# Kernel tuning notes

Measured on AMD Instinct MI355X. Metric: run time of the kernel, lower is better.

Reference implementation:

```python
import jax, jax.numpy as jnp
import numpy as np

N_EMBD = 1024
HEAD_SIZE = 64


def setup_inputs() -> dict:
    key = jax.random.key(0)
    ks = jax.random.split(key, 7)
    B, T, C, H = 4, 4096, N_EMBD, HEAD_SIZE
    s = 1.0 / np.sqrt(C)
    return {
        "x": jax.random.normal(ks[0], (B, T, C), dtype=jnp.float32),
        "Wk": jax.random.uniform(ks[1], (C, H), jnp.float32, -s, s),
        "bk": jax.random.uniform(ks[2], (H,), jnp.float32, -s, s),
        "Wq": jax.random.uniform(ks[3], (C, H), jnp.float32, -s, s),
        "bq": jax.random.uniform(ks[4], (H,), jnp.float32, -s, s),
        "Wv": jax.random.uniform(ks[5], (C, H), jnp.float32, -s, s),
        "bv": jax.random.uniform(ks[6], (H,), jnp.float32, -s, s),
    }


def reference(x, Wk, bk, Wq, bq, Wv, bv):
    B, T, C = x.shape
    k = x @ Wk + bk  # [B,T,H]
    q = x @ Wq + bq
    v = x @ Wv + bv
    scale = k.shape[-1] ** -0.5
    wei = jnp.einsum("bth,bsh->bts", q, k) * scale  # [B,T,T]
    causal = jnp.tril(jnp.ones((T, T), dtype=bool))
    wei = jnp.where(causal, wei, -jnp.inf)
    wei = jax.nn.softmax(wei, axis=-1)
    return jnp.einsum("bts,bsh->bth", wei, v)
```

## Files before the change

kernel.cpp:

```cpp
#include <hip/hip_runtime.h>
#include <hip/hip_bf16.h>


typedef _Float16 f16;
typedef f16 half4 __attribute__((ext_vector_type(4)));
typedef f16 half8 __attribute__((ext_vector_type(8)));
typedef float f32x4 __attribute__((ext_vector_type(4)));

#define T_SEQ 4096
#define QSCL 0.1803368801111204f

__device__ __forceinline__ f32x4 mfma16(half8 a, half8 b, f32x4 c) {
    return __builtin_amdgcn_mfma_f32_16x16x32_f16(a, b, c, 0, 0, 0);
}

__global__ __launch_bounds__(256) void prep_w(const float* __restrict__ Wq,
                                              const float* __restrict__ Wk,
                                              const float* __restrict__ Wv,
                                              f16* __restrict__ Wfrag) {
    int nt = blockIdx.x;
    int mat = nt >> 2;
    const float* W = (mat == 0) ? Wq : (mat == 1 ? Wk : Wv);
    float s = (mat == 0) ? QSCL : 1.0f;
    int tid = threadIdx.x;
    int lane = tid & 63, g = lane >> 4, c16 = lane & 15;
    int ksb = (tid >> 6) * 8;
    int h = ((nt & 3) << 4) + c16;
#pragma unroll
    for (int q = 0; q < 8; ++q) {
        int ks = ksb + q;
        half8 o;
#pragma unroll
        for (int j = 0; j < 8; ++j) {
            int k = ks * 32 + g * 8 + j;
            o[j] = (f16)(W[(size_t)k * 64 + h] * s);
        }
        *reinterpret_cast<half8*>(&Wfrag[((size_t)(nt * 32 + ks) * 64 + lane) * 8]) = o;
    }
}

__global__ __launch_bounds__(256, 4) void proj(const float* __restrict__ x,
                                               const f16* __restrict__ Wfrag,
                                               const float* __restrict__ bk,
                                               const float* __restrict__ bq,
                                               const float* __restrict__ bv,
                                               f16* __restrict__ Qb, f16* __restrict__ Kb,
                                               f16* __restrict__ Vbt) {
    __shared__ f16 xs[16][1032];
    int m0 = blockIdx.x << 4;
    int tid = threadIdx.x;
    int w = tid >> 6, lane = tid & 63, g = lane >> 4, c16 = lane & 15;
    {
        int row = tid >> 4;
        int c0 = (tid & 15) << 2;
        const float* xr = &x[(size_t)(m0 + row) * 1024 + c0];
#pragma unroll
        for (int chunk = 0; chunk < 8; ++chunk) {
            float4 A = *reinterpret_cast<const float4*>(xr + chunk * 128);
            float4 B = *reinterpret_cast<const float4*>(xr + chunk * 128 + 64);
            half4 ha, hb;
            ha[0] = (f16)A.x; ha[1] = (f16)A.y; ha[2] = (f16)A.z; ha[3] = (f16)A.w;
            hb[0] = (f16)B.x; hb[1] = (f16)B.y; hb[2] = (f16)B.z; hb[3] = (f16)B.w;
            *reinterpret_cast<half4*>(&xs[row][c0 + chunk * 128]) = ha;
            *reinterpret_cast<half4*>(&xs[row][c0 + chunk * 128 + 64]) = hb;
        }
    }
    __syncthreads();
    f32x4 zero = {0.f, 0.f, 0.f, 0.f};
    f32x4 acc[3];
#pragma unroll
    for (int i = 0; i < 3; ++i) acc[i] = zero;
    const f16* wbase = &Wfrag[(size_t)(w * 3) * 32 * 64 * 8 + (size_t)lane * 8];
#pragma unroll 8
    for (int ks = 0; ks < 32; ++ks) {
        half8 a = *reinterpret_cast<const half8*>(&xs[c16][ks * 32 + g * 8]);
#pragma unroll
        for (int i = 0; i < 3; ++i) {
            half8 bf = *reinterpret_cast<const half8*>(
                wbase + ((size_t)i * 32 + ks) * 64 * 8);
            acc[i] = mfma16(a, bf, acc[i]);
        }
    }
    int b = m0 >> 12;
#pragma unroll
    for (int i = 0; i < 3; ++i) {
        int nt = w * 3 + i;
        int mat = nt >> 2;
        int h = ((nt & 3) << 4) + c16;
        float bias = (mat == 0) ? bq[h] * QSCL : (mat == 1 ? bk[h] : bv[h]);
#pragma unroll
        for (int j = 0; j < 4; ++j) {
            int row = m0 + g * 4 + j;
            f16 val = (f16)(acc[i][j] + bias);
            if (mat == 0) Qb[(size_t)row * 64 + h] = val;
            else if (mat == 1) Kb[(size_t)row * 64 + h] = val;
            else Vbt[((size_t)(b * 64 + h)) * 4096 + (row & 4095)] = val;
        }
    }
}

__global__ __launch_bounds__(256) void attn(const f16* __restrict__ Qb,
                                            const f16* __restrict__ Kb,
                                            const f16* __restrict__ Vbt,
                                            f16* __restrict__ Opart,
                                            float* __restrict__ Ml) {
    int rem = 287 - (int)blockIdx.x;
    int qt = 0, ck = 0;
    for (int bd = 0; bd < 8; ++bd) {
        int cnt = 8 * (bd + 1);
        if (rem < cnt) { qt = bd * 8 + rem / (bd + 1); ck = rem % (bd + 1); break; }
        rem -= cnt;
    }
    int b = blockIdx.y;
    int t0 = ck << 3;
    int nIter = min(8, qt + 1 - t0);
    int q0 = qt << 6;
    const f16* Q = Qb + (size_t)b * T_SEQ * 64;
    const f16* K = Kb + (size_t)b * T_SEQ * 64;
    const f16* Vg = Vbt + (size_t)b * 64 * T_SEQ;
    int tid = threadIdx.x;
    int w = tid >> 6, lane = tid & 63, g = lane >> 4, c16 = lane & 15;
    __shared__ f16 Kt[2][64][72];
    __shared__ f16 Vt[2][64][72];
    __shared__ f16 Pl[4][16][72];

    int qr = q0 + 16 * w + c16;
    half8 qf0 = *reinterpret_cast<const half8*>(&Q[(size_t)qr * 64 + g * 8]);
    half8 qf1 = *reinterpret_cast<const half8*>(&Q[(size_t)qr * 64 + 32 + g * 8]);

    f32x4 zero = {0.f, 0.f, 0.f, 0.f};
    f32x4 oacc[4];
#pragma unroll
    for (int i = 0; i < 4; ++i) oacc[i] = zero;
    float m_run = -__builtin_inff(), l_run = 0.f;

    int sr = tid >> 2, sc = (tid & 3) << 4;
    int k0 = t0 << 6;
    half8 kr0 = *reinterpret_cast<const half8*>(&K[(size_t)(k0 + sr) * 64 + sc]);
    half8 kr1 = *reinterpret_cast<const half8*>(&K[(size_t)(k0 + sr) * 64 + sc + 8]);
    half8 vr0 = *reinterpret_cast<const half8*>(&Vg[(size_t)sr * T_SEQ + k0 + sc]);
    half8 vr1 = *reinterpret_cast<const half8*>(&Vg[(size_t)sr * T_SEQ + k0 + sc + 8]);
    *reinterpret_cast<half8*>(&Kt[0][sr][sc]) = kr0;
    *reinterpret_cast<half8*>(&Kt[0][sr][sc + 8]) = kr1;
    *reinterpret_cast<half8*>(&Vt[0][sr][sc]) = vr0;
    *reinterpret_cast<half8*>(&Vt[0][sr][sc + 8]) = vr1;
    __syncthreads();
    int cur = 0;

    for (int it = 0; it < nIter; ++it) {
        int gt = t0 + it;
        if (it + 1 < nIter) {
            int kn = (gt + 1) << 6;
            kr0 = *reinterpret_cast<const half8*>(&K[(size_t)(kn + sr) * 64 + sc]);
            kr1 = *reinterpret_cast<const half8*>(&K[(size_t)(kn + sr) * 64 + sc + 8]);
            vr0 = *reinterpret_cast<const half8*>(&Vg[(size_t)sr * T_SEQ + kn + sc]);
            vr1 = *reinterpret_cast<const half8*>(&Vg[(size_t)sr * T_SEQ + kn + sc + 8]);
        }
        f32x4 st[4];
#pragma unroll
        for (int nt = 0; nt < 4; ++nt) st[nt] = zero;
#pragma unroll
        for (int nt = 0; nt < 4; ++nt) {
            half8 kf0 = *reinterpret_cast<const half8*>(&Kt[cur][nt * 16 + c16][g * 8]);
            half8 kf1 = *reinterpret_cast<const half8*>(&Kt[cur][nt * 16 + c16][32 + g * 8]);
            st[nt] = mfma16(kf0, qf0, st[nt]);
            st[nt] = mfma16(kf1, qf1, st[nt]);
        }
        if (gt == qt) {
            int kb = gt << 6;
#pragma unroll
            for (int nt = 0; nt < 4; ++nt)
#pragma unroll
                for (int jj = 0; jj < 4; ++jj)
                    if (kb + nt * 16 + g * 4 + jj > qr) st[nt][jj] = -1e30f;
        }
        float mx;
        {
            f32x4 e01 = __builtin_elementwise_max(st[0], st[1]);
            f32x4 e23 = __builtin_elementwise_max(st[2], st[3]);
            f32x4 e = __builtin_elementwise_max(e01, e23);
            mx = fmaxf(fmaxf(e[0], e[1]), fmaxf(e[2], e[3]));
        }
        mx = fmaxf(mx, __shfl_xor(mx, 16, 64));
        mx = fmaxf(mx, __shfl_xor(mx, 32, 64));
        float nm = fmaxf(m_run, mx);
        float al = exp2f(m_run - nm);
        m_run = nm;
        float rs = 0.f;
#pragma unroll
        for (int nt = 0; nt < 4; ++nt) {
            float s0 = exp2f(st[nt][0] - m_run);
            float s1 = exp2f(st[nt][1] - m_run);
            float s2 = exp2f(st[nt][2] - m_run);
            float s3 = exp2f(st[nt][3] - m_run);
            st[nt][0] = s0; st[nt][1] = s1; st[nt][2] = s2; st[nt][3] = s3;
            rs += (s0 + s1) + (s2 + s3);
        }
        rs += __shfl_xor(rs, 16, 64);
        rs += __shfl_xor(rs, 32, 64);
        l_run = l_run * al + rs;
#pragma unroll
        for (int ht = 0; ht < 4; ++ht)
#pragma unroll
            for (int jj = 0; jj < 4; ++jj) oacc[ht][jj] *= al;
#pragma unroll
        for (int nt = 0; nt < 4; ++nt) {
            half4 p4;
            p4[0] = (f16)st[nt][0]; p4[1] = (f16)st[nt][1];
            p4[2] = (f16)st[nt][2]; p4[3] = (f16)st[nt][3];
            *reinterpret_cast<half4*>(&Pl[w][c16][nt * 16 + g * 4]) = p4;
        }
        half8 pa0 = *reinterpret_cast<const half8*>(&Pl[w][c16][g * 8]);
        half8 pa1 = *reinterpret_cast<const half8*>(&Pl[w][c16][32 + g * 8]);
#pragma unroll
        for (int ht = 0; ht < 4; ++ht) {
            half8 vb0 = *reinterpret_cast<const half8*>(&Vt[cur][ht * 16 + c16][g * 8]);
            half8 vb1 = *reinterpret_cast<const half8*>(&Vt[cur][ht * 16 + c16][32 + g * 8]);
            oacc[ht] = mfma16(vb0, pa0, oacc[ht]);
            oacc[ht] = mfma16(vb1, pa1, oacc[ht]);
        }
        if (it + 1 < nIter) {
            *reinterpret_cast<half8*>(&Kt[cur ^ 1][sr][sc]) = kr0;
            *reinterpret_cast<half8*>(&Kt[cur ^ 1][sr][sc + 8]) = kr1;
            *reinterpret_cast<half8*>(&Vt[cur ^ 1][sr][sc]) = vr0;
            *reinterpret_cast<half8*>(&Vt[cur ^ 1][sr][sc + 8]) = vr1;
        }
        __syncthreads();
        cur ^= 1;
    }
    int slot = (((b << 6) + qt) << 3) + ck;
    f16* Op = Opart + (size_t)slot * 4096;
    float* mlp = Ml + (size_t)slot * 128;
    int r = 16 * w + c16;
#pragma unroll
    for (int ht = 0; ht < 4; ++ht) {
        half4 o4;
        o4[0] = (f16)oacc[ht][0]; o4[1] = (f16)oacc[ht][1];
        o4[2] = (f16)oacc[ht][2]; o4[3] = (f16)oacc[ht][3];
        *reinterpret_cast<half4*>(&Op[r * 64 + ht * 16 + g * 4]) = o4;
    }
    if (g == 0) { mlp[r] = m_run; mlp[64 + r] = l_run; }
}

__global__ __launch_bounds__(256) void combine(const f16* __restrict__ Opart,
                                               const float* __restrict__ Ml,
                                               float* __restrict__ out) {
    int qt = blockIdx.x, b = blockIdx.y;
    int nck = (qt >> 3) + 1;
    int tid = threadIdx.x;
    int row = tid >> 2, c0 = (tid & 3) << 4;
    int bslot = ((b << 6) + qt) << 3;
    float mv[8], lv[8];
    float M = -1e30f;
#pragma unroll
    for (int i = 0; i < 8; ++i)
        if (i < nck) {
            mv[i] = Ml[(size_t)(bslot + i) * 128 + row];
            lv[i] = Ml[(size_t)(bslot + i) * 128 + 64 + row];
            M = fmaxf(M, mv[i]);
        }
    float L = 0.f, sc[8];
#pragma unroll
    for (int i = 0; i < 8; ++i)
        if (i < nck) { sc[i] = exp2f(mv[i] - M); L += lv[i] * sc[i]; }
    float inv = 1.0f / L;
    float o[16];
#pragma unroll
    for (int j = 0; j < 16; ++j) o[j] = 0.f;
#pragma unroll
    for (int i = 0; i < 8; ++i)
        if (i < nck) {
            const f16* Op = Opart + (size_t)(bslot + i) * 4096 + row * 64 + c0;
            half8 h0 = *reinterpret_cast<const half8*>(Op);
            half8 h1 = *reinterpret_cast<const half8*>(Op + 8);
#pragma unroll
            for (int j = 0; j < 8; ++j) {
                o[j] += sc[i] * (float)h0[j];
                o[8 + j] += sc[i] * (float)h1[j];
            }
        }
    float* op = &out[((size_t)b * T_SEQ + (qt << 6) + row) * 64 + c0];
#pragma unroll
    for (int j = 0; j < 16; ++j) op[j] = o[j] * inv;
}

extern "C" void kernel_launch(void* const* d_in, const int* in_sizes, int n_in,
                              void* d_out, int out_size, void* d_ws, size_t ws_size,
                              hipStream_t stream) {
    (void)in_sizes; (void)n_in; (void)out_size; (void)ws_size;
    const float* x  = (const float*)d_in[0];
    const float* Wk = (const float*)d_in[1];
    const float* bk = (const float*)d_in[2];
    const float* Wq = (const float*)d_in[3];
    const float* bq = (const float*)d_in[4];
    const float* Wv = (const float*)d_in[5];
    const float* bv = (const float*)d_in[6];
    float* out = (float*)d_out;
    char* ws = (char*)d_ws;
    f16* Wfrag = (f16*)(ws);
    f16* Qb    = (f16*)(ws + 393216);
    f16* Kb    = (f16*)(ws + 393216 + 2097152);
    f16* Vbt   = (f16*)(ws + 393216 + 2 * 2097152);
    f16* Opart = (f16*)(ws + 393216 + 3 * 2097152);
    float* Ml  = (float*)(ws + 393216 + 3 * 2097152 + 16777216);

    prep_w<<<12, 256, 0, stream>>>(Wq, Wk, Wv, Wfrag);
    proj<<<1024, 256, 0, stream>>>(x, Wfrag, bk, bq, bv, Qb, Kb, Vbt);
    attn<<<dim3(288, 4), 256, 0, stream>>>(Qb, Kb, Vbt, Opart, Ml);
    combine<<<dim3(64, 4), 256, 0, stream>>>(Opart, Ml, out);
}
```

Measured before the change: 157.6 us.

## Process two query tiles per attention block to reuse K/V tiles

Each attention block now handles a pair of adjacent 64-row query tiles, sharing each K/V tile loaded into shared memory between both, with key chunks cut from 8 to 4 tiles. The work decomposition, partial-result slot layout (16 chunks per query tile) and combine kernel change to match. This halves K/V global/LDS traffic per query row, at the cost of more registers (two accumulator sets, two Q fragments), more partial outputs and a larger combine. Launch goes from 288 to 272 blocks per batch.

Result: slower. 169.1 us (+7.4%).

```diff
diff --git a/kernel.cpp b/kernel.cpp
--- a/kernel.cpp
+++ b/kernel.cpp
@@ -104,17 +104,23 @@
                                             const f16* __restrict__ Vbt,
                                             f16* __restrict__ Opart,
                                             float* __restrict__ Ml) {
-    int rem = 287 - (int)blockIdx.x;
-    int qt = 0, ck = 0;
-    for (int bd = 0; bd < 8; ++bd) {
-        int cnt = 8 * (bd + 1);
-        if (rem < cnt) { qt = bd * 8 + rem / (bd + 1); ck = rem % (bd + 1); break; }
+    int rem = 271 - (int)blockIdx.x;
+    int qtp = 0, ck = 0;
+#pragma unroll
+    for (int m = 0; m < 16; ++m) {
+        int cnt = 2 * (m + 1);
+        if (rem < cnt) {
+            if (rem >= m + 1) { qtp = 2 * m + 1; ck = rem - (m + 1); }
+            else { qtp = 2 * m; ck = rem; }
+            break;
+        }
         rem -= cnt;
     }
+    int qtA = qtp * 2, qtB = qtp * 2 + 1;
     int b = blockIdx.y;
-    int t0 = ck << 3;
-    int nIter = min(8, qt + 1 - t0);
-    int q0 = qt << 6;
+    int t0 = ck << 2;
+    int nIter = min(4, qtB - t0 + 1);
+    int q0A = qtA << 6, q0B = qtB << 6;
     const f16* Q = Qb + (size_t)b * T_SEQ * 64;
     const f16* K = Kb + (size_t)b * T_SEQ * 64;
     const f16* Vg = Vbt + (size_t)b * 64 * T_SEQ;
@@ -124,15 +130,18 @@
     __shared__ f16 Vt[2][64][72];
     __shared__ f16 Pl[4][16][72];
 
-    int qr = q0 + 16 * w + c16;
-    half8 qf0 = *reinterpret_cast<const half8*>(&Q[(size_t)qr * 64 + g * 8]);
-    half8 qf1 = *reinterpret_cast<const half8*>(&Q[(size_t)qr * 64 + 32 + g * 8]);
+    int qrA = q0A + 16 * w + c16, qrB = q0B + 16 * w + c16;
+    half8 qfA0 = *reinterpret_cast<const half8*>(&Q[(size_t)qrA * 64 + g * 8]);
+    half8 qfA1 = *reinterpret_cast<const half8*>(&Q[(size_t)qrA * 64 + 32 + g * 8]);
+    half8 qfB0 = *reinterpret_cast<const half8*>(&Q[(size_t)qrB * 64 + g * 8]);
+    half8 qfB1 = *reinterpret_cast<const half8*>(&Q[(size_t)qrB * 64 + 32 + g * 8]);
 
     f32x4 zero = {0.f, 0.f, 0.f, 0.f};
-    f32x4 oacc[4];
-#pragma unroll
-    for (int i = 0; i < 4; ++i) oacc[i] = zero;
-    float m_run = -__builtin_inff(), l_run = 0.f;
+    f32x4 oaccA[4], oaccB[4];
+#pragma unroll
+    for (int i = 0; i < 4; ++i) { oaccA[i] = zero; oaccB[i] = zero; }
+    float mA = -__builtin_inff(), lA = 0.f;
+    float mB = -__builtin_inff(), lB = 0.f;
 
     int sr = tid >> 2, sc = (tid & 3) << 4;
     int k0 = t0 << 6;
@@ -149,6 +158,7 @@
 
     for (int it = 0; it < nIter; ++it) {
         int gt = t0 + it;
+        bool doA = (gt <= qtA);
         if (it + 1 < nIter) {
             int kn = (gt + 1) << 6;
             kr0 = *reinterpret_cast<const half8*>(&K[(size_t)(kn + sr) * 64 + sc]);
@@ -156,68 +166,128 @@
             vr0 = *reinterpret_cast<const half8*>(&Vg[(size_t)sr * T_SEQ + kn + sc]);
             vr1 = *reinterpret_cast<const half8*>(&Vg[(size_t)sr * T_SEQ + kn + sc + 8]);
         }
-        f32x4 st[4];
-#pragma unroll
-        for (int nt = 0; nt < 4; ++nt) st[nt] = zero;
+        f32x4 sA[4], sB[4];
+#pragma unroll
+        for (int nt = 0; nt < 4; ++nt) { sA[nt] = zero; sB[nt] = zero; }
 #pragma unroll
         for (int nt = 0; nt < 4; ++nt) {
             half8 kf0 = *reinterpret_cast<const half8*>(&Kt[cur][nt * 16 + c16][g * 8]);
             half8 kf1 = *reinterpret_cast<const half8*>(&Kt[cur][nt * 16 + c16][32 + g * 8]);
-            st[nt] = mfma16(kf0, qf0, st[nt]);
-            st[nt] = mfma16(kf1, qf1, st[nt]);
-        }
-        if (gt == qt) {
-            int kb = gt << 6;
-#pragma unroll
-            for (int nt = 0; nt < 4; ++nt)
-#pragma unroll
-                for (int jj = 0; jj < 4; ++jj)
-                    if (kb + nt * 16 + g * 4 + jj > qr) st[nt][jj] = -1e30f;
-        }
-        float mx;
+            sB[nt] = mfma16(kf0, qfB0, sB[nt]);
+            sB[nt] = mfma16(kf1, qfB1, sB[nt]);
+            if (doA) {
+                sA[nt] = mfma16(kf0, qfA0, sA[nt]);
+                sA[nt] = mfma16(kf1, qfA1, sA[nt]);
+            }
+        }
+        int kb = gt << 6;
+        if (doA) {
+            if (gt == qtA) {
+#pragma unroll
+                for (int nt = 0; nt < 4; ++nt)
+#pragma unroll
+                    for (int jj = 0; jj < 4; ++jj)
+                        if (kb + nt * 16 + g * 4 + jj > qrA) sA[nt][jj] = -1e30f;
+            }
+            float mx;
+            {
+                f32x4 e = __builtin_elementwise_max(
+                    __builtin_elementwise_max(sA[0], sA[1]),
+                    __builtin_elementwise_max(sA[2], sA[3]));
+                mx = fmaxf(fmaxf(e[0], e[1]), fmaxf(e[2], e[3]));
+            }
+            mx = fmaxf(mx, __shfl_xor(mx, 16, 64));
+            mx = fmaxf(mx, __shfl_xor(mx, 32, 64));
+            float nm = fmaxf(mA, mx);
+            float al = exp2f(mA - nm);
+            mA = nm;
+            float rs = 0.f;
+#pragma unroll
+            for (int nt = 0; nt < 4; ++nt) {
+                float s0 = exp2f(sA[nt][0] - mA);
+                float s1 = exp2f(sA[nt][1] - mA);
+                float s2 = exp2f(sA[nt][2] - mA);
+                float s3 = exp2f(sA[nt][3] - mA);
+                sA[nt][0] = s0; sA[nt][1] = s1; sA[nt][2] = s2; sA[nt][3] = s3;
+                rs += (s0 + s1) + (s2 + s3);
+            }
+            rs += __shfl_xor(rs, 16, 64);
+            rs += __shfl_xor(rs, 32, 64);
+            lA = lA * al + rs;
+#pragma unroll
+            for (int ht = 0; ht < 4; ++ht)
+#pragma unroll
+                for (int jj = 0; jj < 4; ++jj) oaccA[ht][jj] *= al;
+#pragma unroll
+            for (int nt = 0; nt < 4; ++nt) {
+                half4 p4;
+                p4[0] = (f16)sA[nt][0]; p4[1] = (f16)sA[nt][1];
+                p4[2] = (f16)sA[nt][2]; p4[3] = (f16)sA[nt][3];
+                *reinterpret_cast<half4*>(&Pl[w][c16][nt * 16 + g * 4]) = p4;
+            }
+            half8 pa0 = *reinterpret_cast<const half8*>(&Pl[w][c16][g * 8]);
+            half8 pa1 = *reinterpret_cast<const half8*>(&Pl[w][c16][32 + g * 8]);
+#pragma unroll
+            for (int ht = 0; ht < 4; ++ht) {
+                half8 vb0 = *reinterpret_cast<const half8*>(&Vt[cur][ht * 16 + c16][g * 8]);
+                half8 vb1 = *reinterpret_cast<const half8*>(&Vt[cur][ht * 16 + c16][32 + g * 8]);
+                oaccA[ht] = mfma16(vb0, pa0, oaccA[ht]);
+                oaccA[ht] = mfma16(vb1, pa1, oaccA[ht]);
+            }
+        }
         {
-            f32x4 e01 = __builtin_elementwise_max(st[0], st[1]);
-            f32x4 e23 = __builtin_elementwise_max(st[2], st[3]);
-            f32x4 e = __builtin_elementwise_max(e01, e23);
-            mx = fmaxf(fmaxf(e[0], e[1]), fmaxf(e[2], e[3]));
-        }
-        mx = fmaxf(mx, __shfl_xor(mx, 16, 64));
-        mx = fmaxf(mx, __shfl_xor(mx, 32, 64));
-        float nm = fmaxf(m_run, mx);
-        float al = exp2f(m_run - nm);
-        m_run = nm;
-        float rs = 0.f;
-#pragma unroll
-        for (int nt = 0; nt < 4; ++nt) {
-            float s0 = exp2f(st[nt][0] - m_run);
-            float s1 = exp2f(st[nt][1] - m_run);
-            float s2 = exp2f(st[nt][2] - m_run);
-            float s3 = exp2f(st[nt][3] - m_run);
-            st[nt][0] = s0; st[nt][1] = s1; st[nt][2] = s2; st[nt][3] = s3;
-            rs += (s0 + s1) + (s2 + s3);
-        }
-        rs += __shfl_xor(rs, 16, 64);
-        rs += __shfl_xor(rs, 32, 64);
-        l_run = l_run * al + rs;
-#pragma unroll
-        for (int ht = 0; ht < 4; ++ht)
-#pragma unroll
-            for (int jj = 0; jj < 4; ++jj) oacc[ht][jj] *= al;
-#pragma unroll
-        for (int nt = 0; nt < 4; ++nt) {
-            half4 p4;
-            p4[0] = (f16)st[nt][0]; p4[1] = (f16)st[nt][1];
-            p4[2] = (f16)st[nt][2]; p4[3] = (f16)st[nt][3];
-            *reinterpret_cast<half4*>(&Pl[w][c16][nt * 16 + g * 4]) = p4;
-        }
-        half8 pa0 = *reinterpret_cast<const half8*>(&Pl[w][c16][g * 8]);
-        half8 pa1 = *reinterpret_cast<const half8*>(&Pl[w][c16][32 + g * 8]);
-#pragma unroll
-        for (int ht = 0; ht < 4; ++ht) {
-            half8 vb0 = *reinterpret_cast<const half8*>(&Vt[cur][ht * 16 + c16][g * 8]);
-            half8 vb1 = *reinterpret_cast<const half8*>(&Vt[cur][ht * 16 + c16][32 + g * 8]);
-            oacc[ht] = mfma16(vb0, pa0, oacc[ht]);
-            oacc[ht] = mfma16(vb1, pa1, oacc[ht]);
+            if (gt == qtB) {
+#pragma unroll
+                for (int nt = 0; nt < 4; ++nt)
+#pragma unroll
+                    for (int jj = 0; jj < 4; ++jj)
+                        if (kb + nt * 16 + g * 4 + jj > qrB) sB[nt][jj] = -1e30f;
+            }
+            float mx;
+            {
+                f32x4 e = __builtin_elementwise_max(
+                    __builtin_elementwise_max(sB[0], sB[1]),
+                    __builtin_elementwise_max(sB[2], sB[3]));
+                mx = fmaxf(fmaxf(e[0], e[1]), fmaxf(e[2], e[3]));
+            }
+            mx = fmaxf(mx, __shfl_xor(mx, 16, 64));
+            mx = fmaxf(mx, __shfl_xor(mx, 32, 64));
+            float nm = fmaxf(mB, mx);
+            float al = exp2f(mB - nm);
+            mB = nm;
+            float rs = 0.f;
+#pragma unroll
+            for (int nt = 0; nt < 4; ++nt) {
+                float s0 = exp2f(sB[nt][0] - mB);
+                float s1 = exp2f(sB[nt][1] - mB);
+                float s2 = exp2f(sB[nt][2] - mB);
+                float s3 = exp2f(sB[nt][3] - mB);
+                sB[nt][0] = s0; sB[nt][1] = s1; sB[nt][2] = s2; sB[nt][3] = s3;
+                rs += (s0 + s1) + (s2 + s3);
+            }
+            rs += __shfl_xor(rs, 16, 64);
+            rs += __shfl_xor(rs, 32, 64);
+            lB = lB * al + rs;
+#pragma unroll
+            for (int ht = 0; ht < 4; ++ht)
+#pragma unroll
+                for (int jj = 0; jj < 4; ++jj) oaccB[ht][jj] *= al;
+#pragma unroll
+            for (int nt = 0; nt < 4; ++nt) {
+                half4 p4;
+                p4[0] = (f16)sB[nt][0]; p4[1] = (f16)sB[nt][1];
+                p4[2] = (f16)sB[nt][2]; p4[3] = (f16)sB[nt][3];
+                *reinterpret_cast<half4*>(&Pl[w][c16][nt * 16 + g * 4]) = p4;
+            }
+            half8 pa0 = *reinterpret_cast<const half8*>(&Pl[w][c16][g * 8]);
+            half8 pa1 = *reinterpret_cast<const half8*>(&Pl[w][c16][32 + g * 8]);
+#pragma unroll
+            for (int ht = 0; ht < 4; ++ht) {
+                half8 vb0 = *reinterpret_cast<const half8*>(&Vt[cur][ht * 16 + c16][g * 8]);
+                half8 vb1 = *reinterpret_cast<const half8*>(&Vt[cur][ht * 16 + c16][32 + g * 8]);
+                oaccB[ht] = mfma16(vb0, pa0, oaccB[ht]);
+                oaccB[ht] = mfma16(vb1, pa1, oaccB[ht]);
+            }
         }
         if (it + 1 < nIter) {
             *reinterpret_cast<half8*>(&Kt[cur ^ 1][sr][sc]) = kr0;
@@ -228,47 +298,62 @@
         __syncthreads();
         cur ^= 1;
     }
-    int slot = (((b << 6) + qt) << 3) + ck;
-    f16* Op = Opart + (size_t)slot * 4096;
-    float* mlp = Ml + (size_t)slot * 128;
     int r = 16 * w + c16;
-#pragma unroll
-    for (int ht = 0; ht < 4; ++ht) {
-        half4 o4;
-        o4[0] = (f16)oacc[ht][0]; o4[1] = (f16)oacc[ht][1];
-        o4[2] = (f16)oacc[ht][2]; o4[3] = (f16)oacc[ht][3];
-        *reinterpret_cast<half4*>(&Op[r * 64 + ht * 16 + g * 4]) = o4;
-    }
-    if (g == 0) { mlp[r] = m_run; mlp[64 + r] = l_run; }
+    {
+        int slot = (((b << 6) + qtA) << 4) + ck;
+        f16* Op = Opart + (size_t)slot * 4096;
+        float* mlp = Ml + (size_t)slot * 128;
+#pragma unroll
+        for (int ht = 0; ht < 4; ++ht) {
+            half4 o4;
+            o4[0] = (f16)oaccA[ht][0]; o4[1] = (f16)oaccA[ht][1];
+            o4[2] = (f16)oaccA[ht][2]; o4[3] = (f16)oaccA[ht][3];
+            *reinterpret_cast<half4*>(&Op[r * 64 + ht * 16 + g * 4]) = o4;
+        }
+        if (g == 0) { mlp[r] = mA; mlp[64 + r] = lA; }
+    }
+    {
+        int slot = (((b << 6) + qtB) << 4) + ck;
+        f16* Op = Opart + (size_t)slot * 4096;
+        float* mlp = Ml + (size_t)slot * 128;
+#pragma unroll
+        for (int ht = 0; ht < 4; ++ht) {
+            half4 o4;
+            o4[0] = (f16)oaccB[ht][0]; o4[1] = (f16)oaccB[ht][1];
+            o4[2] = (f16)oaccB[ht][2]; o4[3] = (f16)oaccB[ht][3];
+            *reinterpret_cast<half4*>(&Op[r * 64 + ht * 16 + g * 4]) = o4;
+        }
+        if (g == 0) { mlp[r] = mB; mlp[64 + r] = lB; }
+    }
 }
 
 __global__ __launch_bounds__(256) void combine(const f16* __restrict__ Opart,
                                                const float* __restrict__ Ml,
                                                float* __restrict__ out) {
     int qt = blockIdx.x, b = blockIdx.y;
-    int nck = (qt >> 3) + 1;
+    int nck = (qt >> 2) + 1;
     int tid = threadIdx.x;
     int row = tid >> 2, c0 = (tid & 3) << 4;
-    int bslot = ((b << 6) + qt) << 3;
-    float mv[8], lv[8];
+    int bslot = ((b << 6) + qt) << 4;
     float M = -1e30f;
-#pragma unroll
-    for (int i = 0; i < 8; ++i)
+    float mv[16], lv[16];
+#pragma unroll
+    for (int i = 0; i < 16; ++i)
         if (i < nck) {
             mv[i] = Ml[(size_t)(bslot + i) * 128 + row];
             lv[i] = Ml[(size_t)(bslot + i) * 128 + 64 + row];
             M = fmaxf(M, mv[i]);
         }
-    float L = 0.f, sc[8];
-#pragma unroll
-    for (int i = 0; i < 8; ++i)
+    float L = 0.f, sc[16];
+#pragma unroll
+    for (int i = 0; i < 16; ++i)
         if (i < nck) { sc[i] = exp2f(mv[i] - M); L += lv[i] * sc[i]; }
     float inv = 1.0f / L;
     float o[16];
 #pragma unroll
     for (int j = 0; j < 16; ++j) o[j] = 0.f;
 #pragma unroll
-    for (int i = 0; i < 8; ++i)
+    for (int i = 0; i < 16; ++i)
         if (i < nck) {
             const f16* Op = Opart + (size_t)(bslot + i) * 4096 + row * 64 + c0;
             half8 h0 = *reinterpret_cast<const half8*>(Op);
@@ -302,10 +387,10 @@
     f16* Kb    = (f16*)(ws + 393216 + 2097152);
     f16* Vbt   = (f16*)(ws + 393216 + 2 * 2097152);
     f16* Opart = (f16*)(ws + 393216 + 3 * 2097152);
-    float* Ml  = (float*)(ws + 393216 + 3 * 2097152 + 16777216);
+    float* Ml  = (float*)(ws + 393216 + 3 * 2097152 + 33554432);
 
     prep_w<<<12, 256, 0, stream>>>(Wq, Wk, Wv, Wfrag);
     proj<<<1024, 256, 0, stream>>>(x, Wfrag, bk, bq, bv, Qb, Kb, Vbt);
-    attn<<<dim3(288, 4), 256, 0, stream>>>(Qb, Kb, Vbt, Opart, Ml);
+    attn<<<dim3(272, 4), 256, 0, stream>>>(Qb, Kb, Vbt, Opart, Ml);
     combine<<<dim3(64, 4), 256, 0, stream>>>(Opart, Ml, out);
 }
```
